# Performance work log

Measured on AMD Instinct MI355X. Metric: run time of the kernel, lower is better.

## Reference

```python
import jax, jax.numpy as jnp
import numpy as np

N = 4096    # nodes per graph
C = 128     # in_channels == out_channels
HEAD = 1
E = 65536   # edges per graph (avg degree 16)


def setup_inputs() -> dict:
    key = jax.random.key(0)
    ks = jax.random.split(key, 24)
    def w(k, shape):
        return jax.random.normal(k, shape, dtype=jnp.float32) * 0.05
    return {
        "x1": jax.random.normal(ks[0], (N, C), dtype=jnp.float32),
        "x2": jax.random.normal(ks[1], (N, C), dtype=jnp.float32),
        "edge_index1": jax.random.randint(ks[2], (2, E), 0, N),
        "edge_index2": jax.random.randint(ks[3], (2, E), 0, N),
        "wl1_w": w(ks[4], (HEAD * C, C)), "wl1_b": w(ks[5], (HEAD * C,)),
        "wr1_w": w(ks[6], (HEAD * C, C)), "wr1_b": w(ks[7], (HEAD * C,)),
        "al1": w(ks[8], (HEAD, C)), "ar1": w(ks[9], (HEAD, C)),
        "wl2_w": w(ks[10], (HEAD * C, C)), "wl2_b": w(ks[11], (HEAD * C,)),
        "wr2_w": w(ks[12], (HEAD * C, C)), "wr2_b": w(ks[13], (HEAD * C,)),
        "al2": w(ks[14], (HEAD, C)), "ar2": w(ks[15], (HEAD, C)),
        "w1_w": w(ks[16], (C, 2 * C)), "w1_b": w(ks[17], (C,)),
        "w2_w": w(ks[18], (C, 2 * C)), "w2_b": w(ks[19], (C,)),
        "lin_w": w(ks[20], (HEAD * C, C)), "lin_b": w(ks[21], (HEAD * C,)),
    }


def _leaky_relu(x):
    return jnp.where(x > 0, x, 0.2 * x)


def _attention(src, tgt, wl, bl, wr, br, al, ar):
    # alpha_l: (N_src,), alpha_r: (N_tot,) -> dense (N_src, N_tot) softmax
    a_l = ((src @ wl.T + bl).reshape(-1, HEAD, C) * al[None]).sum(-1).mean(1)
    a_r = ((tgt @ wr.T + br).reshape(-1, HEAD, C) * ar[None]).sum(-1).mean(1)
    return jax.nn.softmax(_leaky_relu(a_l[:, None] + a_r[None, :]), axis=1)


def _aggr_update(x_i, tgt_all, ei, wl, bl, wr, br, al, ar, ww, wb):
    att = _attention(x_i, tgt_all, wl, bl, wr, br, al, ar)   # (N_i, N_tot)
    ot = x_i - att @ tgt_all                                  # (N_i, C)
    feat = jnp.concatenate([x_i, ot], axis=1)                 # (N_i, 2C)
    n = x_i.shape[0]
    loops = jnp.arange(n)                                     # add_self_loops
    src = jnp.concatenate([ei[0], loops])
    dst = jnp.concatenate([ei[1], loops])
    sums = jax.ops.segment_sum(feat[dst], src, num_segments=n)
    cnt = jax.ops.segment_sum(jnp.ones((src.shape[0],), feat.dtype), src, num_segments=n)
    aggr = sums / cnt[:, None]                                # scatter 'mean'
    return jax.nn.relu(aggr) @ ww.T + wb


def reference(x1, x2, edge_index1, edge_index2,
              wl1_w, wl1_b, wr1_w, wr1_b, al1, ar1,
              wl2_w, wl2_b, wr2_w, wr2_b, al2, ar2,
              w1_w, w1_b, w2_w, w2_b, lin_w, lin_b):
    Xs = [x1, x2]
    eis = [edge_index1, edge_index2]
    layers = [(wl1_w, wl1_b, wr1_w, wr1_b, al1, ar1, w1_w, w1_b),
              (wl2_w, wl2_b, wr2_w, wr2_b, al2, ar2, w2_w, w2_b)]
    for (wl, bl, wr, br, al, ar, ww, wb) in layers:
        tgt = jnp.concatenate(Xs, axis=0)
        Xs = [_aggr_update(Xs[i], tgt, eis[i], wl, bl, wr, br, al, ar, ww, wb)
              for i in range(2)]
    feats = jnp.concatenate(Xs, axis=0) @ lin_w.T + lin_b     # (2N, C)
    return jax.nn.sigmoid(feats @ feats.T)                    # (2N, 2N)
```

## Files before the change

### kernel.cpp

```cpp
#include <hip/hip_runtime.h>
#include <hip/hip_bf16.h>

#define NT 8192
#define NN 4096
#define CD 128
#define NE 65536

typedef __attribute__((ext_vector_type(8))) short bf16x8;
typedef __attribute__((ext_vector_type(16))) float f32x16;
typedef __attribute__((ext_vector_type(4))) float f32x4;

__global__ __launch_bounds__(256) void k_prep(
    const float* __restrict__ x1, const float* __restrict__ x2, float* __restrict__ X,
    const float* __restrict__ W1, const float* __restrict__ W2, const float* __restrict__ WL,
    float* __restrict__ WT1, float* __restrict__ WT2, float* __restrict__ WTL,
    const float* __restrict__ wlw0, const float* __restrict__ wlb0,
    const float* __restrict__ wrw0, const float* __restrict__ wrb0,
    const float* __restrict__ al0, const float* __restrict__ ar0,
    const float* __restrict__ wlw1, const float* __restrict__ wlb1,
    const float* __restrict__ wrw1, const float* __restrict__ wrb1,
    const float* __restrict__ al1, const float* __restrict__ ar1,
    float* __restrict__ VP, int* __restrict__ DEG) {
  int b = blockIdx.x, tid = threadIdx.x;
  int gid = b * 256 + tid;
  {
    const f32x4* s1 = (const f32x4*)x1;
    const f32x4* s2 = (const f32x4*)x2;
    f32x4* d = (f32x4*)X;
    d[gid] = s1[gid];
    d[gid + NN * CD / 4] = s2[gid];
  }
  if (gid < 81920) {
    int idx = gid;
    if (idx < 32768) { int c = idx >> 8, k = idx & 255; WT1[k * 128 + c] = W1[idx]; }
    else if (idx < 65536) { int j = idx - 32768; int c = j >> 8, k = j & 255; WT2[k * 128 + c] = W2[j]; }
    else { int j = idx - 65536; int c = j >> 7, k = j & 127; WTL[k * 128 + c] = WL[j]; }
  }
  if ((b == 508 || b == 509) && tid < 128) {
    int L = b - 508;
    const float* wlw = L ? wlw1 : wlw0;
    const float* wlb = L ? wlb1 : wlb0;
    const float* wrw = L ? wrw1 : wrw0;
    const float* wrb = L ? wrb1 : wrb0;
    const float* alv = L ? al1 : al0;
    const float* arv = L ? ar1 : ar0;
    float* vp = VP + L * 258;
    int c = tid;
    float sl = 0.f, sr = 0.f;
    for (int h = 0; h < 128; ++h) {
      sl += wlw[h * 128 + c] * alv[h];
      sr += wrw[h * 128 + c] * arv[h];
    }
    vp[c] = sl;
    vp[128 + c] = sr;
    if (c < 2) {
      const float* bb = c ? wrb : wlb;
      const float* aa = c ? arv : alv;
      float s = 0.f;
      for (int h = 0; h < 128; ++h) s += bb[h] * aa[h];
      vp[256 + c] = s;
    }
  }
  if (gid < 2 * NN) DEG[gid] = 0;
}

__device__ inline void alar_row(const float* __restrict__ X, const float* __restrict__ VP,
                                float* __restrict__ AL, float* __restrict__ AR,
                                int row, int lane) {
  float x0 = X[row * 128 + lane], x1 = X[row * 128 + 64 + lane];
  float sl = x0 * VP[lane] + x1 * VP[64 + lane];
  float sr = x0 * VP[128 + lane] + x1 * VP[192 + lane];
  #pragma unroll
  for (int m = 1; m < 64; m <<= 1) {
    sl += __shfl_xor(sl, m, 64);
    sr += __shfl_xor(sr, m, 64);
  }
  if (lane == 0) { AL[row] = sl + VP[256]; AR[row] = sr + VP[257]; }
}

__device__ void rank_body(int rb, int tid, const float* __restrict__ AR,
                          int* __restrict__ RANK) {
  __shared__ float tile[1024];
  int jb = rb & 31, tb = rb >> 5;
  int base = tb * 1024;
  for (int t = tid; t < 1024; t += 256) tile[t] = AR[base + t];
  __syncthreads();
  int j = jb * 256 + tid;
  float aj = AR[j];
  int cnt = 0;
  #pragma unroll 8
  for (int u = 0; u < 1024; ++u) {
    float a2 = tile[u];
    cnt += (a2 < aj || (a2 == aj && (base + u) < j)) ? 1 : 0;
  }
  atomicAdd(&RANK[j], cnt);
}

__device__ void scanoff_body(int g, int tid, const int* __restrict__ DEG,
                             int* __restrict__ OFFS, int* __restrict__ CURS) {
  __shared__ int part[256];
  int loc[16];
  int s = 0;
  #pragma unroll
  for (int i = 0; i < 16; ++i) { loc[i] = s; s += DEG[g * NN + tid * 16 + i]; }
  part[tid] = s;
  __syncthreads();
  for (int d = 1; d < 256; d <<= 1) {
    int v = part[tid];
    int o = (tid >= d) ? part[tid - d] : 0;
    __syncthreads();
    part[tid] = v + o;
    __syncthreads();
  }
  int excl = tid ? part[tid - 1] : 0;
  #pragma unroll
  for (int i = 0; i < 16; ++i) {
    int o = excl + loc[i];
    OFFS[g * (NN + 1) + tid * 16 + i] = o;
    CURS[g * NN + tid * 16 + i] = o;
  }
  if (tid == 255) OFFS[g * (NN + 1) + NN] = part[255];
}

__global__ __launch_bounds__(256) void k_s2(
    const int* __restrict__ EI1, const int* __restrict__ EI2, int* __restrict__ DEG,
    const float* __restrict__ X, const float* __restrict__ VP0,
    float* __restrict__ AL, float* __restrict__ AR, int* __restrict__ RANK) {
  int b = blockIdx.x, tid = threadIdx.x;
  if (b < 512) {
    int gid = b * 256 + tid;
    int g = gid >> 16, e = gid & 65535;
    const int* src = g ? EI2 : EI1;
    atomicAdd(&DEG[g * NN + src[e]], 1);
  } else {
    int bb = b - 512;
    if (bb < 32) RANK[bb * 256 + tid] = 0;
    alar_row(X, VP0, AL, AR, bb * 4 + (tid >> 6), tid & 63);
  }
}

__global__ __launch_bounds__(256) void k_s3(
    const int* __restrict__ DEG, int* __restrict__ OFFS, int* __restrict__ CURS,
    const float* __restrict__ AR, int* __restrict__ RANK) {
  int b = blockIdx.x, tid = threadIdx.x;
  if (b < 2) scanoff_body(b, tid, DEG, OFFS, CURS);
  else rank_body(b - 2, tid, AR, RANK);
}

__global__ __launch_bounds__(256) void k_s4(
    const int* __restrict__ EI1, const int* __restrict__ EI2,
    int* __restrict__ CURS, int* __restrict__ ADJ,
    const int* __restrict__ RANK, const float* __restrict__ AR,
    int* __restrict__ PERM, float* __restrict__ ARS) {
  int b = blockIdx.x, tid = threadIdx.x;
  if (b < 512) {
    int gid = b * 256 + tid;
    int g = gid >> 16, e = gid & 65535;
    const int* ei = g ? EI2 : EI1;
    int s = ei[e], d = ei[NE + e];
    int pos = atomicAdd(&CURS[g * NN + s], 1);
    ADJ[g * NE + pos] = d;
  } else {
    int j = (b - 512) * 256 + tid;
    int r = RANK[j];
    PERM[r] = j;
    ARS[r] = AR[j];
  }
}

__global__ void k_rank(const float* __restrict__ AR, int* __restrict__ RANK) {
  rank_body(blockIdx.x, threadIdx.x, AR, RANK);
}
__global__ void k_perm(const int* __restrict__ RANK, const float* __restrict__ AR,
                       int* __restrict__ PERM, float* __restrict__ ARS) {
  int j = blockIdx.x * 256 + threadIdx.x;
  int r = RANK[j];
  PERM[r] = j;
  ARS[r] = AR[j];
}

__global__ __launch_bounds__(256) void k_scanA(
    const float* __restrict__ X, const int* __restrict__ PERM,
    const float* __restrict__ ARS, int* __restrict__ RANK,
    float* __restrict__ P1, float* __restrict__ P2,
    float* __restrict__ CT1, float* __restrict__ CT2,
    float* __restrict__ Q1L, float* __restrict__ Q2L,
    float* __restrict__ QCT1, float* __restrict__ QCT2) {
  __shared__ int pc[64];
  __shared__ float w[2][64];
  __shared__ float part[2][4][32];
  __shared__ float qpart[2][4];
  int b = blockIdx.x;
  if (b < 32) RANK[b * 256 + threadIdx.x] = 0;
  int chunk = b >> 2, sub = b & 3;
  int tid = threadIdx.x;
  int a = tid >> 7;
  int g = (tid >> 5) & 3;
  int cl = tid & 31;
  int c = sub * 32 + cl;
  if (tid < 64) {
    int r = chunk * 64 + tid;
    pc[tid] = PERM[r];
    float ar = ARS[r];
    w[0][tid] = __expf(ar);
    w[1][tid] = __expf(0.2f * ar);
  }
  __syncthreads();
  int t0 = g * 16;
  float loc[16];
  float acc = 0.f;
  #pragma unroll 4
  for (int t = 0; t < 16; ++t) {
    acc += w[a][t0 + t] * X[pc[t0 + t] * 128 + c];
    loc[t] = acc;
  }
  part[a][g][cl] = acc;
  float qloc[16];
  float qacc = 0.f;
  bool doQ = (sub == 0 && cl == 0);
  if (doQ) {
    for (int t = 0; t < 16; ++t) { qacc += w[a][t0 + t]; qloc[t] = qacc; }
    qpart[a][g] = qacc;
  }
  __syncthreads();
  float off = (g > 0 ? part[a][0][cl] : 0.f) + (g > 1 ? part[a][1][cl] : 0.f) +
              (g > 2 ? part[a][2][cl] : 0.f);
  float* P = a ? P2 : P1;
  #pragma unroll 4
  for (int t = 0; t < 16; ++t) P[(chunk * 64 + t0 + t) * 128 + c] = loc[t] + off;
  if (g == 3) (a ? CT2 : CT1)[chunk * 128 + c] = off + acc;
  if (doQ) {
    float qoff = (g > 0 ? qpart[a][0] : 0.f) + (g > 1 ? qpart[a][1] : 0.f) +
                 (g > 2 ? qpart[a][2] : 0.f);
    float* Q = a ? Q2L : Q1L;
    for (int t = 0; t < 16; ++t) Q[chunk * 64 + t0 + t] = qloc[t] + qoff;
    if (g == 3) (a ? QCT2 : QCT1)[chunk] = qoff + qacc;
  }
}

__global__ __launch_bounds__(320) void k_scanB(
    const float* __restrict__ CT1, const float* __restrict__ CT2,
    const float* __restrict__ QCT1, const float* __restrict__ QCT2,
    float* __restrict__ OFF1, float* __restrict__ OFF2,
    float* __restrict__ QOF1, float* __restrict__ QOF2) {
  int tid = threadIdx.x;
  if (tid < 128) {
    float acc = 0.f;
    #pragma unroll 8
    for (int ch = 0; ch < 128; ++ch) { acc += CT1[ch * 128 + tid]; OFF1[ch * 128 + tid] = acc; }
  } else if (tid < 256) {
    int c = tid - 128;
    float acc = 0.f;
    #pragma unroll 8
    for (int ch = 0; ch < 128; ++ch) { acc += CT2[ch * 128 + c]; OFF2[ch * 128 + c] = acc; }
  } else if (tid == 256) {
    float acc = 0.f;
    for (int ch = 0; ch < 128; ++ch) { acc += QCT1[ch]; QOF1[ch] = acc; }
  } else if (tid == 257) {
    float acc = 0.f;
    for (int ch = 0; ch < 128; ++ch) { acc += QCT2[ch]; QOF2[ch] = acc; }
  }
}

__global__ void k_combine(const float* __restrict__ X, const float* __restrict__ AL,
                          const float* __restrict__ ARS,
                          const float* __restrict__ P1, const float* __restrict__ P2,
                          const float* __restrict__ OFF1, const float* __restrict__ OFF2,
                          const float* __restrict__ Q1L, const float* __restrict__ Q2L,
                          const float* __restrict__ QOF1, const float* __restrict__ QOF2,
                          float* __restrict__ OT) {
  int row = blockIdx.x * 2 + (threadIdx.x >> 7);
  int c = threadIdx.x & 127;
  float ali = AL[row];
  float A1 = __expf(ali), A2 = __expf(0.2f * ali);
  float xv = -ali;
  int lo = 0, hi = NT;
  while (lo < hi) {
    int mid = (lo + hi) >> 1;
    if (ARS[mid] <= xv) lo = mid + 1; else hi = mid;
  }
  int b = lo - 1;
  float p1 = 0.f, p2 = 0.f, q1 = 0.f, q2 = 0.f;
  if (b >= 0) {
    int ch = b >> 6;
    p1 = P1[b * 128 + c] + (ch ? OFF1[(ch - 1) * 128 + c] : 0.f);
    p2 = P2[b * 128 + c] + (ch ? OFF2[(ch - 1) * 128 + c] : 0.f);
    q1 = Q1L[b] + (ch ? QOF1[ch - 1] : 0.f);
    q2 = Q2L[b] + (ch ? QOF2[ch - 1] : 0.f);
  }
  float T1 = OFF1[127 * 128 + c];
  float QT1 = QOF1[127];
  float num = A1 * (T1 - p1) + A2 * p2;
  float den = A1 * (QT1 - q1) + A2 * q2;
  OT[row * 128 + c] = X[row * 128 + c] - num / den;
}

__global__ __launch_bounds__(256) void k_ag(
    const float* __restrict__ X, const float* __restrict__ OT,
    const int* __restrict__ OFFS, const int* __restrict__ ADJ,
    const float* __restrict__ WT, const float* __restrict__ WB, float* __restrict__ XN,
    int mode,
    const float* __restrict__ VP1, float* __restrict__ AL, float* __restrict__ AR,
    const float* __restrict__ WTL, const float* __restrict__ LINB,
    __hip_bfloat16* __restrict__ FBF) {
  __shared__ float sA[8 * 256];
  __shared__ float sB[8 * 128];
  int b = blockIdx.x, tid = threadIdx.x;
  int lane = tid & 63, wv = tid >> 6, c4 = lane & 31;
  {
    int beg[2], end[2];
    const f32x4* srcp[2];
    const int* adjp[2];
    f32x4 acc[2];
    #pragma unroll
    for (int k = 0; k < 2; ++k) {
      int node = b * 8 + wv * 2 + k;
      int g = node >> 12, n = node & (NN - 1);
      beg[k] = OFFS[g * (NN + 1) + n];
      end[k] = OFFS[g * (NN + 1) + n + 1];
      srcp[k] = (const f32x4*)((lane < 32 ? X : OT) + (size_t)g * NN * CD);
      adjp[k] = ADJ + g * NE;
      acc[k] = srcp[k][n * 32 + c4];
    }
    int maxd = max(end[0] - beg[0], end[1] - beg[1]);
    for (int s = 0; s < maxd; ++s) {
      #pragma unroll
      for (int k = 0; k < 2; ++k) {
        if (beg[k] + s < end[k]) acc[k] += srcp[k][adjp[k][beg[k] + s] * 32 + c4];
      }
    }
    #pragma unroll
    for (int k = 0; k < 2; ++k) {
      f32x4 r = acc[k] / (float)(end[k] - beg[k] + 1);
      #pragma unroll
      for (int q = 0; q < 4; ++q) r[q] = fmaxf(r[q], 0.f);
      *(f32x4*)&sA[(wv * 2 + k) * 256 + (lane < 32 ? c4 * 4 : 128 + c4 * 4)] = r;
    }
  }
  __syncthreads();
  int c = tid & 127, half = tid >> 7;
  float accv[4];
  float bc = WB[c];
  #pragma unroll
  for (int i = 0; i < 4; ++i) accv[i] = bc;
  for (int k4 = 0; k4 < 64; ++k4) {
    float w0 = WT[(k4 * 4 + 0) * 128 + c];
    float w1v = WT[(k4 * 4 + 1) * 128 + c];
    float w2v = WT[(k4 * 4 + 2) * 128 + c];
    float w3 = WT[(k4 * 4 + 3) * 128 + c];
    #pragma unroll
    for (int i = 0; i < 4; ++i) {
      f32x4 av = *(const f32x4*)&sA[(half * 4 + i) * 256 + k4 * 4];
      accv[i] += av[0] * w0 + av[1] * w1v + av[2] * w2v + av[3] * w3;
    }
  }
  #pragma unroll
  for (int i = 0; i < 4; ++i) {
    sB[(half * 4 + i) * 128 + c] = accv[i];
    if (mode == 0) XN[(size_t)(b * 8 + half * 4 + i) * 128 + c] = accv[i];
  }
  __syncthreads();
  if (mode == 0) {
    #pragma unroll
    for (int k = 0; k < 2; ++k) {
      int lr = wv * 2 + k;
      float x0 = sB[lr * 128 + lane], x1 = sB[lr * 128 + 64 + lane];
      float sl = x0 * VP1[lane] + x1 * VP1[64 + lane];
      float sr = x0 * VP1[128 + lane] + x1 * VP1[192 + lane];
      #pragma unroll
      for (int m = 1; m < 64; m <<= 1) {
        sl += __shfl_xor(sl, m, 64);
        sr += __shfl_xor(sr, m, 64);
      }
      if (lane == 0) { AL[b * 8 + lr] = sl + VP1[256]; AR[b * 8 + lr] = sr + VP1[257]; }
    }
  } else {
    float acl[4];
    float lb = LINB[c];
    #pragma unroll
    for (int i = 0; i < 4; ++i) acl[i] = lb;
    for (int k4 = 0; k4 < 32; ++k4) {
      float w0 = WTL[(k4 * 4 + 0) * 128 + c];
      float w1v = WTL[(k4 * 4 + 1) * 128 + c];
      float w2v = WTL[(k4 * 4 + 2) * 128 + c];
      float w3 = WTL[(k4 * 4 + 3) * 128 + c];
      #pragma unroll
      for (int i = 0; i < 4; ++i) {
        f32x4 av = *(const f32x4*)&sB[(half * 4 + i) * 128 + k4 * 4];
        acl[i] += av[0] * w0 + av[1] * w1v + av[2] * w2v + av[3] * w3;
      }
    }
    #pragma unroll
    for (int i = 0; i < 4; ++i)
      FBF[(size_t)(b * 8 + half * 4 + i) * 128 + c] = __float2bfloat16(acl[i]);
  }
}

__device__ inline f32x16 zero16() {
  f32x16 v;
  #pragma unroll
  for (int i = 0; i < 16; ++i) v[i] = 0.f;
  return v;
}

__device__ inline float sigf(float v) {
  return __builtin_amdgcn_rcpf(1.f + __expf(-v));
}

__global__ __launch_bounds__(256) void k_final(const unsigned short* __restrict__ F,
                                               float* __restrict__ out) {
  __shared__ __align__(16) char smem[65536];
  unsigned short* AT = (unsigned short*)smem;
  unsigned short* BT = AT + 16384;
  int cb = blockIdx.x, rb = blockIdx.y;
  int tid = threadIdx.x;
  #pragma unroll
  for (int q = 0; q < 8; ++q) {
    int idx = q * 256 + tid;
    int r = idx >> 4, ck = idx & 15;
    unsigned off = (unsigned)((r * 256 + ck * 16) ^ ((r & 7) << 4));
    uint4 va = *(const uint4*)(F + (size_t)(rb * 128 + r) * 128 + ck * 8);
    *(uint4*)((char*)AT + off) = va;
    uint4 vb = *(const uint4*)(F + (size_t)(cb * 128 + r) * 128 + ck * 8);
    *(uint4*)((char*)BT + off) = vb;
  }
  __syncthreads();
  int lane = tid & 63, w = tid >> 6;
  int wr = w >> 1, wc = w & 1;
  int l31 = lane & 31, kh = lane >> 5;
  int xorm = (l31 & 7) << 4;
  int rowA0 = wr * 64 + l31, rowA1 = rowA0 + 32;
  int rowB0 = wc * 64 + l31, rowB1 = rowB0 + 32;
  f32x16 a00 = zero16(), a01 = zero16(), a10 = zero16(), a11 = zero16();
  #pragma unroll
  for (int ks = 0; ks < 8; ++ks) {
    int kb = ks * 32 + kh * 16;
    bf16x8 av0 = *(const bf16x8*)((const char*)AT + ((rowA0 * 256 + kb) ^ xorm));
    bf16x8 av1 = *(const bf16x8*)((const char*)AT + ((rowA1 * 256 + kb) ^ xorm));
    bf16x8 bv0 = *(const bf16x8*)((const char*)BT + ((rowB0 * 256 + kb) ^ xorm));
    bf16x8 bv1 = *(const bf16x8*)((const char*)BT + ((rowB1 * 256 + kb) ^ xorm));
    a00 = __builtin_amdgcn_mfma_f32_32x32x16_bf16(av0, bv0, a00, 0, 0, 0);
    a01 = __builtin_amdgcn_mfma_f32_32x32x16_bf16(av0, bv1, a01, 0, 0, 0);
    a10 = __builtin_amdgcn_mfma_f32_32x32x16_bf16(av1, bv0, a10, 0, 0, 0);
    a11 = __builtin_amdgcn_mfma_f32_32x32x16_bf16(av1, bv1, a11, 0, 0, 0);
  }
  __syncthreads();
  float* lw = (float*)smem + w * 4096;
  #pragma unroll
  for (int r = 0; r < 16; ++r) {
    int rl = (r & 3) + 8 * (r >> 2) + 4 * kh;
    lw[rl * 64 + l31] = sigf(a00[r]);
    lw[rl * 64 + l31 + 32] = sigf(a01[r]);
    lw[(rl + 32) * 64 + l31] = sigf(a10[r]);
    lw[(rl + 32) * 64 + l31 + 32] = sigf(a11[r]);
  }
  int grb = rb * 128 + wr * 64, gcb = cb * 128 + wc * 64;
  #pragma unroll
  for (int j = 0; j < 16; ++j) {
    int row = j * 4 + (lane >> 4);
    int c4 = (lane & 15) * 4;
    f32x4 v = *(const f32x4*)&lw[row * 64 + c4];
    *(f32x4*)&out[(size_t)(grb + row) * 8192 + gcb + c4] = v;
  }
}

extern "C" void kernel_launch(void* const* d_in, const int* in_sizes, int n_in,
                              void* d_out, int out_size, void* d_ws, size_t ws_size,
                              hipStream_t stream) {
  (void)in_sizes; (void)n_in; (void)out_size; (void)ws_size;
  const float* x1 = (const float*)d_in[0];
  const float* x2 = (const float*)d_in[1];
  const int* ei1 = (const int*)d_in[2];
  const int* ei2 = (const int*)d_in[3];
  const float* wl_w[2] = {(const float*)d_in[4], (const float*)d_in[10]};
  const float* wl_b[2] = {(const float*)d_in[5], (const float*)d_in[11]};
  const float* wr_w[2] = {(const float*)d_in[6], (const float*)d_in[12]};
  const float* wr_b[2] = {(const float*)d_in[7], (const float*)d_in[13]};
  const float* alv[2] = {(const float*)d_in[8], (const float*)d_in[14]};
  const float* arv[2] = {(const float*)d_in[9], (const float*)d_in[15]};
  const float* ww_w[2] = {(const float*)d_in[16], (const float*)d_in[18]};
  const float* ww_b[2] = {(const float*)d_in[17], (const float*)d_in[19]};
  const float* lin_w = (const float*)d_in[20];
  const float* lin_b = (const float*)d_in[21];

  char* wp = (char*)d_ws;
  auto alloc = [&](size_t b) -> char* {
    char* p = wp;
    wp += (b + 255) & ~(size_t)255;
    return p;
  };
  float* XA = (float*)alloc((size_t)NT * CD * 4);
  float* XB = (float*)alloc((size_t)NT * CD * 4);
  float* OT = (float*)alloc((size_t)NT * CD * 4);
  float* P1 = (float*)alloc((size_t)NT * CD * 4);
  float* P2 = (float*)alloc((size_t)NT * CD * 4);
  __hip_bfloat16* FBF = (__hip_bfloat16*)alloc((size_t)NT * CD * 2);
  float* CT1 = (float*)alloc(128 * 128 * 4);
  float* CT2 = (float*)alloc(128 * 128 * 4);
  float* OFF1 = (float*)alloc(128 * 128 * 4);
  float* OFF2 = (float*)alloc(128 * 128 * 4);
  float* AL = (float*)alloc(NT * 4);
  float* AR_ = (float*)alloc(NT * 4);
  float* ARS = (float*)alloc(NT * 4);
  float* Q1L = (float*)alloc(NT * 4);
  float* Q2L = (float*)alloc(NT * 4);
  float* QCT1 = (float*)alloc(128 * 4);
  float* QCT2 = (float*)alloc(128 * 4);
  float* QOF1 = (float*)alloc(128 * 4);
  float* QOF2 = (float*)alloc(128 * 4);
  float* VP = (float*)alloc(2 * 258 * 4);
  float* WT1 = (float*)alloc(256 * 128 * 4);
  float* WT2 = (float*)alloc(256 * 128 * 4);
  float* WTL = (float*)alloc(128 * 128 * 4);
  int* RANK = (int*)alloc(NT * 4);
  int* PERM = (int*)alloc(NT * 4);
  int* DEG = (int*)alloc(2 * NN * 4);
  int* OFFS = (int*)alloc(2 * (NN + 1) * 4);
  int* CURS = (int*)alloc(2 * NN * 4);
  int* ADJ = (int*)alloc(2 * NE * 4);

  k_prep<<<512, 256, 0, stream>>>(x1, x2, XA, ww_w[0], ww_w[1], lin_w, WT1, WT2, WTL,
                                  wl_w[0], wl_b[0], wr_w[0], wr_b[0], alv[0], arv[0],
                                  wl_w[1], wl_b[1], wr_w[1], wr_b[1], alv[1], arv[1],
                                  VP, DEG);
  k_s2<<<2560, 256, 0, stream>>>(ei1, ei2, DEG, XA, VP, AL, AR_, RANK);
  k_s3<<<258, 256, 0, stream>>>(DEG, OFFS, CURS, AR_, RANK);
  k_s4<<<544, 256, 0, stream>>>(ei1, ei2, CURS, ADJ, RANK, AR_, PERM, ARS);
  k_scanA<<<512, 256, 0, stream>>>(XA, PERM, ARS, RANK, P1, P2, CT1, CT2, Q1L, Q2L, QCT1, QCT2);
  k_scanB<<<1, 320, 0, stream>>>(CT1, CT2, QCT1, QCT2, OFF1, OFF2, QOF1, QOF2);
  k_combine<<<4096, 256, 0, stream>>>(XA, AL, ARS, P1, P2, OFF1, OFF2, Q1L, Q2L, QOF1, QOF2, OT);
  k_ag<<<1024, 256, 0, stream>>>(XA, OT, OFFS, ADJ, WT1, ww_b[0], XB,
                                 0, VP + 258, AL, AR_, WTL, lin_b, FBF);
  k_rank<<<256, 256, 0, stream>>>(AR_, RANK);
  k_perm<<<32, 256, 0, stream>>>(RANK, AR_, PERM, ARS);
  k_scanA<<<512, 256, 0, stream>>>(XB, PERM, ARS, RANK, P1, P2, CT1, CT2, Q1L, Q2L, QCT1, QCT2);
  k_scanB<<<1, 320, 0, stream>>>(CT1, CT2, QCT1, QCT2, OFF1, OFF2, QOF1, QOF2);
  k_combine<<<4096, 256, 0, stream>>>(XB, AL, ARS, P1, P2, OFF1, OFF2, Q1L, Q2L, QOF1, QOF2, OT);
  k_ag<<<1024, 256, 0, stream>>>(XB, OT, OFFS, ADJ, WT2, ww_b[1], XB,
                                 1, VP, AL, AR_, WTL, lin_b, FBF);
  k_final<<<dim3(64, 64), 256, 0, stream>>>((const unsigned short*)FBF, (float*)d_out);
}
```

Measured before the change: 299.0 us.

## Interleave x and ot rows, process 16 nodes per aggregation block, halve rank tiles

k_combine now writes a 256-wide interleaved [x | x - att@x] row buffer. k_ag can then gather each neighbour's full feature row with one contiguous 1KB load per wavefront instead of splitting lanes between two arrays. k_ag handles 16 nodes per block (4 per wave) to amortize weight reads in the dense update and expose more gather parallelism, at the cost of more registers and shared memory. The rank kernel tile is halved to 512 with doubled grid, which increases the number of atomics.

```diff
diff --git a/kernel.cpp b/kernel.cpp
--- a/kernel.cpp
+++ b/kernel.cpp
@@ -80,16 +80,16 @@
 
 __device__ void rank_body(int rb, int tid, const float* __restrict__ AR,
                           int* __restrict__ RANK) {
-  __shared__ float tile[1024];
+  __shared__ float tile[512];
   int jb = rb & 31, tb = rb >> 5;
-  int base = tb * 1024;
-  for (int t = tid; t < 1024; t += 256) tile[t] = AR[base + t];
+  int base = tb * 512;
+  for (int t = tid; t < 512; t += 256) tile[t] = AR[base + t];
   __syncthreads();
   int j = jb * 256 + tid;
   float aj = AR[j];
   int cnt = 0;
   #pragma unroll 8
-  for (int u = 0; u < 1024; ++u) {
+  for (int u = 0; u < 512; ++u) {
     float a2 = tile[u];
     cnt += (a2 < aj || (a2 == aj && (base + u) < j)) ? 1 : 0;
   }
@@ -268,7 +268,7 @@
                           const float* __restrict__ OFF1, const float* __restrict__ OFF2,
                           const float* __restrict__ Q1L, const float* __restrict__ Q2L,
                           const float* __restrict__ QOF1, const float* __restrict__ QOF2,
-                          float* __restrict__ OT) {
+                          float* __restrict__ XO) {
   int row = blockIdx.x * 2 + (threadIdx.x >> 7);
   int c = threadIdx.x & 127;
   float ali = AL[row];
@@ -292,78 +292,84 @@
   float QT1 = QOF1[127];
   float num = A1 * (T1 - p1) + A2 * p2;
   float den = A1 * (QT1 - q1) + A2 * q2;
-  OT[row * 128 + c] = X[row * 128 + c] - num / den;
+  float x = X[row * 128 + c];
+  XO[(size_t)row * 256 + c] = x;
+  XO[(size_t)row * 256 + 128 + c] = x - num / den;
 }
 
 __global__ __launch_bounds__(256) void k_ag(
-    const float* __restrict__ X, const float* __restrict__ OT,
+    const float* __restrict__ XO,
     const int* __restrict__ OFFS, const int* __restrict__ ADJ,
     const float* __restrict__ WT, const float* __restrict__ WB, float* __restrict__ XN,
     int mode,
     const float* __restrict__ VP1, float* __restrict__ AL, float* __restrict__ AR,
     const float* __restrict__ WTL, const float* __restrict__ LINB,
     __hip_bfloat16* __restrict__ FBF) {
-  __shared__ float sA[8 * 256];
-  __shared__ float sB[8 * 128];
+  __shared__ float sA[16 * 256];
+  __shared__ float sB[16 * 128];
   int b = blockIdx.x, tid = threadIdx.x;
-  int lane = tid & 63, wv = tid >> 6, c4 = lane & 31;
+  int lane = tid & 63, wv = tid >> 6;
   {
-    int beg[2], end[2];
-    const f32x4* srcp[2];
-    const int* adjp[2];
-    f32x4 acc[2];
-    #pragma unroll
-    for (int k = 0; k < 2; ++k) {
-      int node = b * 8 + wv * 2 + k;
+    int beg[4], end[4], gof[4];
+    const int* adjp[4];
+    f32x4 acc[4];
+    #pragma unroll
+    for (int k = 0; k < 4; ++k) {
+      int node = b * 16 + wv * 4 + k;
       int g = node >> 12, n = node & (NN - 1);
       beg[k] = OFFS[g * (NN + 1) + n];
       end[k] = OFFS[g * (NN + 1) + n + 1];
-      srcp[k] = (const f32x4*)((lane < 32 ? X : OT) + (size_t)g * NN * CD);
       adjp[k] = ADJ + g * NE;
-      acc[k] = srcp[k][n * 32 + c4];
-    }
-    int maxd = max(end[0] - beg[0], end[1] - beg[1]);
+      gof[k] = g * NN;
+      acc[k] = *(const f32x4*)&XO[(size_t)node * 256 + lane * 4];
+    }
+    int maxd = 0;
+    #pragma unroll
+    for (int k = 0; k < 4; ++k) maxd = max(maxd, end[k] - beg[k]);
     for (int s = 0; s < maxd; ++s) {
       #pragma unroll
-      for (int k = 0; k < 2; ++k) {
-        if (beg[k] + s < end[k]) acc[k] += srcp[k][adjp[k][beg[k] + s] * 32 + c4];
+      for (int k = 0; k < 4; ++k) {
+        if (beg[k] + s < end[k]) {
+          int d = adjp[k][beg[k] + s];
+          acc[k] += *(const f32x4*)&XO[(size_t)(gof[k] + d) * 256 + lane * 4];
+        }
       }
     }
     #pragma unroll
-    for (int k = 0; k < 2; ++k) {
+    for (int k = 0; k < 4; ++k) {
       f32x4 r = acc[k] / (float)(end[k] - beg[k] + 1);
       #pragma unroll
       for (int q = 0; q < 4; ++q) r[q] = fmaxf(r[q], 0.f);
-      *(f32x4*)&sA[(wv * 2 + k) * 256 + (lane < 32 ? c4 * 4 : 128 + c4 * 4)] = r;
+      *(f32x4*)&sA[(wv * 4 + k) * 256 + lane * 4] = r;
     }
   }
   __syncthreads();
   int c = tid & 127, half = tid >> 7;
-  float accv[4];
+  float accv[8];
   float bc = WB[c];
   #pragma unroll
-  for (int i = 0; i < 4; ++i) accv[i] = bc;
+  for (int i = 0; i < 8; ++i) accv[i] = bc;
   for (int k4 = 0; k4 < 64; ++k4) {
     float w0 = WT[(k4 * 4 + 0) * 128 + c];
     float w1v = WT[(k4 * 4 + 1) * 128 + c];
     float w2v = WT[(k4 * 4 + 2) * 128 + c];
     float w3 = WT[(k4 * 4 + 3) * 128 + c];
     #pragma unroll
-    for (int i = 0; i < 4; ++i) {
-      f32x4 av = *(const f32x4*)&sA[(half * 4 + i) * 256 + k4 * 4];
+    for (int i = 0; i < 8; ++i) {
+      f32x4 av = *(const f32x4*)&sA[(half * 8 + i) * 256 + k4 * 4];
       accv[i] += av[0] * w0 + av[1] * w1v + av[2] * w2v + av[3] * w3;
     }
   }
   #pragma unroll
-  for (int i = 0; i < 4; ++i) {
-    sB[(half * 4 + i) * 128 + c] = accv[i];
-    if (mode == 0) XN[(size_t)(b * 8 + half * 4 + i) * 128 + c] = accv[i];
+  for (int i = 0; i < 8; ++i) {
+    sB[(half * 8 + i) * 128 + c] = accv[i];
+    if (mode == 0) XN[(size_t)(b * 16 + half * 8 + i) * 128 + c] = accv[i];
   }
   __syncthreads();
   if (mode == 0) {
     #pragma unroll
-    for (int k = 0; k < 2; ++k) {
-      int lr = wv * 2 + k;
+    for (int k = 0; k < 4; ++k) {
+      int lr = wv * 4 + k;
       float x0 = sB[lr * 128 + lane], x1 = sB[lr * 128 + 64 + lane];
       float sl = x0 * VP1[lane] + x1 * VP1[64 + lane];
       float sr = x0 * VP1[128 + lane] + x1 * VP1[192 + lane];
@@ -372,27 +378,27 @@
         sl += __shfl_xor(sl, m, 64);
         sr += __shfl_xor(sr, m, 64);
       }
-      if (lane == 0) { AL[b * 8 + lr] = sl + VP1[256]; AR[b * 8 + lr] = sr + VP1[257]; }
+      if (lane == 0) { AL[b * 16 + lr] = sl + VP1[256]; AR[b * 16 + lr] = sr + VP1[257]; }
     }
   } else {
-    float acl[4];
+    float acl[8];
     float lb = LINB[c];
     #pragma unroll
-    for (int i = 0; i < 4; ++i) acl[i] = lb;
+    for (int i = 0; i < 8; ++i) acl[i] = lb;
     for (int k4 = 0; k4 < 32; ++k4) {
       float w0 = WTL[(k4 * 4 + 0) * 128 + c];
       float w1v = WTL[(k4 * 4 + 1) * 128 + c];
       float w2v = WTL[(k4 * 4 + 2) * 128 + c];
       float w3 = WTL[(k4 * 4 + 3) * 128 + c];
       #pragma unroll
-      for (int i = 0; i < 4; ++i) {
-        f32x4 av = *(const f32x4*)&sB[(half * 4 + i) * 128 + k4 * 4];
+      for (int i = 0; i < 8; ++i) {
+        f32x4 av = *(const f32x4*)&sB[(half * 8 + i) * 128 + k4 * 4];
         acl[i] += av[0] * w0 + av[1] * w1v + av[2] * w2v + av[3] * w3;
       }
     }
     #pragma unroll
-    for (int i = 0; i < 4; ++i)
-      FBF[(size_t)(b * 8 + half * 4 + i) * 128 + c] = __float2bfloat16(acl[i]);
+    for (int i = 0; i < 8; ++i)
+      FBF[(size_t)(b * 16 + half * 8 + i) * 128 + c] = __float2bfloat16(acl[i]);
   }
 }
 
@@ -491,7 +497,7 @@
   };
   float* XA = (float*)alloc((size_t)NT * CD * 4);
   float* XB = (float*)alloc((size_t)NT * CD * 4);
-  float* OT = (float*)alloc((size_t)NT * CD * 4);
+  float* XO = (float*)alloc((size_t)NT * 256 * 4);
   float* P1 = (float*)alloc((size_t)NT * CD * 4);
   float* P2 = (float*)alloc((size_t)NT * CD * 4);
   __hip_bfloat16* FBF = (__hip_bfloat16*)alloc((size_t)NT * CD * 2);
@@ -524,19 +530,19 @@
                                   wl_w[1], wl_b[1], wr_w[1], wr_b[1], alv[1], arv[1],
                                   VP, DEG);
   k_s2<<<2560, 256, 0, stream>>>(ei1, ei2, DEG, XA, VP, AL, AR_, RANK);
-  k_s3<<<258, 256, 0, stream>>>(DEG, OFFS, CURS, AR_, RANK);
+  k_s3<<<514, 256, 0, stream>>>(DEG, OFFS, CURS, AR_, RANK);
   k_s4<<<544, 256, 0, stream>>>(ei1, ei2, CURS, ADJ, RANK, AR_, PERM, ARS);
   k_scanA<<<512, 256, 0, stream>>>(XA, PERM, ARS, RANK, P1, P2, CT1, CT2, Q1L, Q2L, QCT1, QCT2);
   k_scanB<<<1, 320, 0, stream>>>(CT1, CT2, QCT1, QCT2, OFF1, OFF2, QOF1, QOF2);
-  k_combine<<<4096, 256, 0, stream>>>(XA, AL, ARS, P1, P2, OFF1, OFF2, Q1L, Q2L, QOF1, QOF2, OT);
-  k_ag<<<1024, 256, 0, stream>>>(XA, OT, OFFS, ADJ, WT1, ww_b[0], XB,
-                                 0, VP + 258, AL, AR_, WTL, lin_b, FBF);
-  k_rank<<<256, 256, 0, stream>>>(AR_, RANK);
+  k_combine<<<4096, 256, 0, stream>>>(XA, AL, ARS, P1, P2, OFF1, OFF2, Q1L, Q2L, QOF1, QOF2, XO);
+  k_ag<<<512, 256, 0, stream>>>(XO, OFFS, ADJ, WT1, ww_b[0], XB,
+                                0, VP + 258, AL, AR_, WTL, lin_b, FBF);
+  k_rank<<<512, 256, 0, stream>>>(AR_, RANK);
   k_perm<<<32, 256, 0, stream>>>(RANK, AR_, PERM, ARS);
   k_scanA<<<512, 256, 0, stream>>>(XB, PERM, ARS, RANK, P1, P2, CT1, CT2, Q1L, Q2L, QCT1, QCT2);
   k_scanB<<<1, 320, 0, stream>>>(CT1, CT2, QCT1, QCT2, OFF1, OFF2, QOF1, QOF2);
-  k_combine<<<4096, 256, 0, stream>>>(XB, AL, ARS, P1, P2, OFF1, OFF2, Q1L, Q2L, QOF1, QOF2, OT);
-  k_ag<<<1024, 256, 0, stream>>>(XB, OT, OFFS, ADJ, WT2, ww_b[1], XB,
-                                 1, VP, AL, AR_, WTL, lin_b, FBF);
+  k_combine<<<4096, 256, 0, stream>>>(XB, AL, ARS, P1, P2, OFF1, OFF2, Q1L, Q2L, QOF1, QOF2, XO);
+  k_ag<<<512, 256, 0, stream>>>(XO, OFFS, ADJ, WT2, ww_b[1], XB,
+                                1, VP, AL, AR_, WTL, lin_b, FBF);
   k_final<<<dim3(64, 64), 256, 0, stream>>>((const unsigned short*)FBF, (float*)d_out);
 }
```

Result: slower. 313.3 us (+4.8%).
